# Performance work log

Measured on AMD Instinct MI355X. Metric: run time of the kernel, lower is better.

The kernel has to match this reference:

```python
import jax, jax.numpy as jnp
import numpy as np

TEMP = 0.07
BASE_TEMP = 0.07
BANK = 8192
B = 512      # samples per view; features has 2*B rows
D = 128      # feature dim
N_CLASSES = 100


def _l2norm(x, axis=-1):
    return x / jnp.linalg.norm(x, axis=axis, keepdims=True)


def setup_inputs() -> dict:
    key = jax.random.key(0)
    k1, k2, k3, k4, k5 = jax.random.split(key, 5)
    # SupCon features are L2-normalized embeddings; two views stacked: [2B, 1, D]
    features = _l2norm(jax.random.normal(k1, (2 * B, 1, D), jnp.float32))
    label = jax.random.randint(k2, (B,), 0, N_CLASSES)
    # memory banks stored as [D, bank_size] (lightly MemoryBankModule layout)
    bank1 = _l2norm(jax.random.normal(k3, (D, BANK), jnp.float32), axis=0)
    bank2 = _l2norm(jax.random.normal(k4, (D, BANK), jnp.float32), axis=0)
    bank_labels = jax.random.randint(k5, (BANK,), 0, N_CLASSES)
    return {"features": features, "label": label, "bank1": bank1,
            "bank2": bank2, "bank_labels": bank_labels}


def _branch_loss(cf, pos_mask, neg_mask):
    # cf: [N, D] anchor==contrast features
    logits = jnp.matmul(cf, cf.T) / TEMP                       # [N, N]
    logits = logits - jax.lax.stop_gradient(logits.max(axis=1, keepdims=True))
    # denominator: sum of exp(logits) over NEGATIVES only (square(mask-1) mask)
    denom = jnp.log((jnp.exp(logits) * neg_mask).sum(axis=1, keepdims=True))
    log_prob = logits - denom                                  # [N, N]
    mean_log_prob_pos = (pos_mask * log_prob).sum(axis=1) / pos_mask.sum(axis=1)
    return -(TEMP / BASE_TEMP) * mean_log_prob_pos             # [N]


def reference(features, label, bank1, bank2, bank_labels):
    d = features.shape[-1]
    fr = features.reshape(-1, d)                # [2B, D]
    nb = fr.shape[0] // 2
    f1, f2 = fr[:nb], fr[nb:]                   # [B, D] each

    labels_all = jnp.concatenate([bank_labels.reshape(-1, 1),
                                  label.reshape(-1, 1)], axis=0)   # [N, 1]
    same = (labels_all == labels_all.T)                            # [N, N]
    mask = same.astype(fr.dtype)
    n = mask.shape[0]
    self_mask = 1.0 - jnp.eye(n, dtype=fr.dtype)
    pos_mask = mask * self_mask                 # positives excluding self
    neg_mask = jnp.square(mask - 1.0)           # 1 where labels differ

    cf1 = jnp.concatenate([bank2.T, f1], axis=0)   # [N, D]
    cf2 = jnp.concatenate([bank1.T, f2], axis=0)   # [N, D]

    class_loss = (_branch_loss(cf1, pos_mask, neg_mask)
                  + _branch_loss(cf2, pos_mask, neg_mask)) / 2.0
    loss = class_loss.mean()
    return (loss, loss, loss)
```

## Files before the change

kernel.cpp:

```cpp
#include <hip/hip_runtime.h>
#include <math.h>

#define NTOT 8704
#define BANKN 8192
#define NB 512
#define DIM 128
#define INVT (1.0f / 0.07f)
#define C2L 20.6099131801f
#define NCHUNK 17
#define TPC 8
#define BN 64

using short8 = __attribute__((ext_vector_type(8))) short;
using ushort8 = __attribute__((ext_vector_type(8))) unsigned short;
using f32x4 = __attribute__((ext_vector_type(4))) float;

static __device__ __forceinline__ ushort f2bf(float f) {
  union { float f; unsigned u; } v;
  v.f = f;
  unsigned r = v.u + 0x7fffu + ((v.u >> 16) & 1u);
  return (ushort)(r >> 16);
}

static __device__ __forceinline__ float fast_exp2(float x) {
#if __has_builtin(__builtin_amdgcn_exp2f)
  return __builtin_amdgcn_exp2f(x);
#else
  return exp2f(x);
#endif
}

__global__ __launch_bounds__(1024) void prep_kernel(
    const int* __restrict__ bank_labels, const int* __restrict__ label,
    int* __restrict__ inv, int* __restrict__ lo, int* __restrict__ hi,
    float* __restrict__ zp) {
  __shared__ int h[101];
  __shared__ int st[101];
  __shared__ int cur[100];
  const int tid = threadIdx.x;
  for (int i = tid; i < NTOT; i += 1024)
    reinterpret_cast<float4*>(zp)[i] = make_float4(0.f, 0.f, 0.f, 0.f);
  if (tid < 101) h[tid] = 0;
  __syncthreads();
  for (int i = tid; i < NTOT; i += 1024) {
    const int v = (i < BANKN) ? bank_labels[i] : label[i - BANKN];
    atomicAdd(&h[v], 1);
  }
  __syncthreads();
  if (tid == 0) {
    int s = 0;
    for (int c = 0; c < 100; ++c) { st[c] = s; s += h[c]; }
    st[100] = s;
  }
  __syncthreads();
  if (tid < 100) cur[tid] = st[tid];
  __syncthreads();
  for (int i = tid; i < NTOT; i += 1024) {
    const int v = (i < BANKN) ? bank_labels[i] : label[i - BANKN];
    const int p = atomicAdd(&cur[v], 1);
    inv[i] = p;
    lo[p] = st[v];
    hi[p] = st[v + 1];
  }
}

__global__ void pack_kernel(const float* __restrict__ features,
                            const float* __restrict__ bank1,
                            const float* __restrict__ bank2,
                            const int* __restrict__ inv,
                            ushort* __restrict__ cf1b,
                            ushort* __restrict__ cf2b) {
  const int branch = blockIdx.z;
  ushort* __restrict__ dst = branch ? cf2b : cf1b;
  const int tx = threadIdx.x, ty = threadIdx.y;
  const int bx = blockIdx.x, by = blockIdx.y;
  if (bx < 256) {
    const float* __restrict__ src = branch ? bank1 : bank2;
    __shared__ float tile[32][33];
    const int col = bx * 32 + tx;
#pragma unroll
    for (int s = 0; s < 32; s += 8)
      tile[ty + s][tx] = src[(size_t)(by * 32 + ty + s) * BANKN + col];
    __syncthreads();
    const int k = by * 32 + tx;
#pragma unroll
    for (int s = 0; s < 32; s += 8) {
      const int p = inv[bx * 32 + ty + s];
      dst[(size_t)p * DIM + k] = f2bf(tile[tx][ty + s]);
    }
  } else {
    const int j = (bx - 256) * 32 + ty;
#pragma unroll
    for (int s = 0; s < 32; s += 8) {
      const int jr = (bx - 256) * 32 + ty + s;
      const int k = by * 32 + tx;
      const float v = features[(size_t)(branch * NB + jr) * DIM + k];
      const int p = inv[BANKN + jr];
      dst[(size_t)p * DIM + k] = f2bf(v);
    }
    (void)j;
  }
}

__global__ __launch_bounds__(256) void supcon_mfma_kernel(
    const ushort* __restrict__ cf1b, const ushort* __restrict__ cf2b,
    const int* __restrict__ lo, const int* __restrict__ hi,
    float* __restrict__ zp) {
  const int rb = blockIdx.x;
  const int chunk = blockIdx.y;
  const int branch = blockIdx.z;
  const ushort* __restrict__ cf = branch ? cf2b : cf1b;

  const int tid = threadIdx.x;
  const int wid = tid >> 6, lane = tid & 63;
  const int l15 = lane & 15, l4 = lane >> 4;
  const int rowW = rb * 128 + wid * 32;

  __shared__ ushort Bt[2][BN * DIM];

  short8 a[2][4];
#pragma unroll
  for (int rt = 0; rt < 2; ++rt) {
    const int r = rowW + rt * 16 + l15;
#pragma unroll
    for (int ks = 0; ks < 4; ++ks)
      a[rt][ks] = *reinterpret_cast<const short8*>(cf + (size_t)r * DIM + ks * 32 + l4 * 8);
  }
  int rlo[2][4], rhi[2][4];
#pragma unroll
  for (int rt = 0; rt < 2; ++rt)
#pragma unroll
    for (int rg = 0; rg < 4; ++rg) {
      const int rr = rowW + rt * 16 + l4 * 4 + rg;
      rlo[rt][rg] = lo[rr];
      rhi[rt][rg] = hi[rr];
    }
  const int u_lo = lo[rowW];
  const int u_hi = hi[rowW + 31];
  const int lo_last = lo[rowW + 31];
  const int hi_first = hi[rowW];

  float Zr[2][4] = {{0.f, 0.f, 0.f, 0.f}, {0.f, 0.f, 0.f, 0.f}};
  float Pr[2][4] = {{0.f, 0.f, 0.f, 0.f}, {0.f, 0.f, 0.f, 0.f}};

  auto STAGE = [&](int t, int buf) {
    const int col0 = (chunk * TPC + t) * BN;
#pragma unroll
    for (int it = 0; it < 4; ++it) {
      const int o = it * 256 + tid;
      const int row = o >> 4, cc = o & 15;
      const ushort* src =
          cf + (size_t)(col0 + row) * DIM + ((cc ^ (row & 7)) * 8);
      ushort* dst = &Bt[buf][(it * 256 + wid * 64) * 8];
      __builtin_amdgcn_global_load_lds(
          (const __attribute__((address_space(1))) void*)src,
          (__attribute__((address_space(3))) void*)dst, 16, 0, 0);
    }
  };

  STAGE(0, 0);
  asm volatile("s_waitcnt vmcnt(0)" ::: "memory");
  __syncthreads();

  int cur = 0;
  for (int t = 0; t < TPC; ++t) {
    if (t + 1 < TPC) STAGE(t + 1, cur ^ 1);

    const int col0 = (chunk * TPC + t) * BN;

    f32x4 acc[2][4];
#pragma unroll
    for (int rt = 0; rt < 2; ++rt)
#pragma unroll
      for (int ct = 0; ct < 4; ++ct) acc[rt][ct] = (f32x4){0.f, 0.f, 0.f, 0.f};

#pragma unroll
    for (int ks = 0; ks < 4; ++ks) {
      short8 b[4];
#pragma unroll
      for (int ct = 0; ct < 4; ++ct) {
        const int r = ct * 16 + l15;
        const int swz = (ks * 4 + l4) ^ (r & 7);
        b[ct] = *reinterpret_cast<const short8*>(&Bt[cur][r * DIM + swz * 8]);
      }
#pragma unroll
      for (int rt = 0; rt < 2; ++rt)
#pragma unroll
        for (int ct = 0; ct < 4; ++ct)
          acc[rt][ct] = __builtin_amdgcn_mfma_f32_16x16x32_bf16(
              a[rt][ks], b[ct], acc[rt][ct], 0, 0, 0);
    }

    if (col0 + BN <= u_lo || col0 >= u_hi) {
#pragma unroll
      for (int ct = 0; ct < 4; ++ct)
#pragma unroll
        for (int rt = 0; rt < 2; ++rt)
#pragma unroll
          for (int rg = 0; rg < 4; ++rg)
            Zr[rt][rg] += fast_exp2(fmaf(acc[rt][ct][rg], C2L, -C2L));
    } else if (col0 >= lo_last && col0 + BN <= hi_first) {
#pragma unroll
      for (int ct = 0; ct < 4; ++ct)
#pragma unroll
        for (int rt = 0; rt < 2; ++rt)
#pragma unroll
          for (int rg = 0; rg < 4; ++rg) Pr[rt][rg] += acc[rt][ct][rg];
    } else {
#pragma unroll
      for (int ct = 0; ct < 4; ++ct) {
        const int c = col0 + ct * 16 + l15;
#pragma unroll
        for (int rt = 0; rt < 2; ++rt)
#pragma unroll
          for (int rg = 0; rg < 4; ++rg) {
            const float v = acc[rt][ct][rg];
            const float e = fast_exp2(fmaf(v, C2L, -C2L));
            const bool s = (c >= rlo[rt][rg]) && (c < rhi[rt][rg]);
            Zr[rt][rg] += s ? 0.0f : e;
            Pr[rt][rg] += s ? v : 0.0f;
          }
      }
    }

    asm volatile("s_waitcnt vmcnt(0)" ::: "memory");
    __syncthreads();
    cur ^= 1;
  }

  float* Zrow = zp;
  float* Prow = zp + 2 * NTOT;
#pragma unroll
  for (int rt = 0; rt < 2; ++rt)
#pragma unroll
    for (int rg = 0; rg < 4; ++rg) {
      float z = Zr[rt][rg], p = Pr[rt][rg];
#pragma unroll
      for (int off = 1; off < 16; off <<= 1) {
        z += __shfl_xor(z, off);
        p += __shfl_xor(p, off);
      }
      if (l15 == 0) {
        const int row = rowW + rt * 16 + l4 * 4 + rg;
        atomicAdd(&Zrow[branch * NTOT + row], z);
        atomicAdd(&Prow[branch * NTOT + row], p);
      }
    }
}

__global__ __launch_bounds__(1024) void loss_kernel(const float* __restrict__ zp,
                                                    const int* __restrict__ lo,
                                                    const int* __restrict__ hi,
                                                    float* __restrict__ out) {
  const int tid = threadIdx.x;
  const float* Zrow = zp;
  const float* Prow = zp + 2 * NTOT;
  float local = 0.f;
  for (int idx = tid; idx < 2 * NTOT; idx += 1024) {
    const int row = (idx >= NTOT) ? idx - NTOT : idx;
    const float z = Zrow[idx];
    const float p = Prow[idx];
    const float C = (float)(hi[row] - lo[row] - 1);
    const float denom = INVT + logf(z);
    local += -((INVT * (p - 1.0f)) / C - denom);
  }
  __shared__ float s[1024];
  s[tid] = local;
  __syncthreads();
  for (int st = 512; st > 0; st >>= 1) {
    if (tid < st) s[tid] += s[tid + st];
    __syncthreads();
  }
  if (tid == 0) {
    const float v = s[0] / (2.0f * NTOT);
    out[0] = v; out[1] = v; out[2] = v;
  }
}

extern "C" void kernel_launch(void* const* d_in, const int* in_sizes, int n_in,
                              void* d_out, int out_size, void* d_ws,
                              size_t ws_size, hipStream_t stream) {
  const float* features = (const float*)d_in[0];
  const int* label = (const int*)d_in[1];
  const float* bank1 = (const float*)d_in[2];
  const float* bank2 = (const float*)d_in[3];
  const int* bank_labels = (const int*)d_in[4];
  float* out = (float*)d_out;

  char* ws = (char*)d_ws;
  ushort* cf1b = (ushort*)(ws);
  ushort* cf2b = (ushort*)(ws + 2228224);
  int* inv = (int*)(ws + 4456448);
  int* lo = (int*)(ws + 4491264);
  int* hi = (int*)(ws + 4526080);
  float* zp = (float*)(ws + 4560896);

  prep_kernel<<<dim3(1), dim3(1024), 0, stream>>>(bank_labels, label, inv, lo,
                                                  hi, zp);
  pack_kernel<<<dim3(272, DIM / 32, 2), dim3(32, 8), 0, stream>>>(
      features, bank1, bank2, inv, cf1b, cf2b);
  supcon_mfma_kernel<<<dim3(NTOT / 128, NCHUNK, 2), dim3(256), 0, stream>>>(
      cf1b, cf2b, lo, hi, zp);
  loss_kernel<<<dim3(1), dim3(1024), 0, stream>>>(zp, lo, hi, out);
}
```

Baseline: 154.0 us.

## Triple-buffer MFMA tiles, use 2x2 wave grid, and privatize label histograms

The main kernel moves from double to triple buffering with one barrier per tile and a partial vmcnt wait, so the load for tile t+2 is in flight while tile t is computed. Waves now form a 2x2 grid of 64 rows by 32 columns, which lowers LDS B-fragment reads per MFMA. Label bounds now live in shared memory instead of registers, the LDS swizzle widens to 16, and launch bounds request 3 blocks per SM. The prep kernel uses per-wave histograms to reduce atomic contention, at the cost of more LDS and a small prefix step.

```diff
diff --git a/kernel.cpp b/kernel.cpp
--- a/kernel.cpp
+++ b/kernel.cpp
@@ -34,30 +34,46 @@
     const int* __restrict__ bank_labels, const int* __restrict__ label,
     int* __restrict__ inv, int* __restrict__ lo, int* __restrict__ hi,
     float* __restrict__ zp) {
-  __shared__ int h[101];
+  __shared__ int h[16][100];
   __shared__ int st[101];
-  __shared__ int cur[100];
+  __shared__ int tot[100];
   const int tid = threadIdx.x;
+  const int w = tid >> 6;
   for (int i = tid; i < NTOT; i += 1024)
     reinterpret_cast<float4*>(zp)[i] = make_float4(0.f, 0.f, 0.f, 0.f);
-  if (tid < 101) h[tid] = 0;
+  for (int i = tid; i < 1600; i += 1024) (&h[0][0])[i] = 0;
   __syncthreads();
   for (int i = tid; i < NTOT; i += 1024) {
     const int v = (i < BANKN) ? bank_labels[i] : label[i - BANKN];
-    atomicAdd(&h[v], 1);
+    atomicAdd(&h[w][v], 1);
+  }
+  __syncthreads();
+  if (tid < 100) {
+    int s = 0;
+#pragma unroll
+    for (int w2 = 0; w2 < 16; ++w2) s += h[w2][tid];
+    tot[tid] = s;
   }
   __syncthreads();
   if (tid == 0) {
     int s = 0;
-    for (int c = 0; c < 100; ++c) { st[c] = s; s += h[c]; }
+    for (int c = 0; c < 100; ++c) { st[c] = s; s += tot[c]; }
     st[100] = s;
   }
   __syncthreads();
-  if (tid < 100) cur[tid] = st[tid];
+  if (tid < 100) {
+    int base = st[tid];
+#pragma unroll
+    for (int w2 = 0; w2 < 16; ++w2) {
+      const int t = h[w2][tid];
+      h[w2][tid] = base;
+      base += t;
+    }
+  }
   __syncthreads();
   for (int i = tid; i < NTOT; i += 1024) {
     const int v = (i < BANKN) ? bank_labels[i] : label[i - BANKN];
-    const int p = atomicAdd(&cur[v], 1);
+    const int p = atomicAdd(&h[w][v], 1);
     inv[i] = p;
     lo[p] = st[v];
     hi[p] = st[v + 1];
@@ -89,7 +105,6 @@
       dst[(size_t)p * DIM + k] = f2bf(tile[tx][ty + s]);
     }
   } else {
-    const int j = (bx - 256) * 32 + ty;
 #pragma unroll
     for (int s = 0; s < 32; s += 8) {
       const int jr = (bx - 256) * 32 + ty + s;
@@ -98,11 +113,10 @@
       const int p = inv[BANKN + jr];
       dst[(size_t)p * DIM + k] = f2bf(v);
     }
-    (void)j;
-  }
-}
-
-__global__ __launch_bounds__(256) void supcon_mfma_kernel(
+  }
+}
+
+__global__ __launch_bounds__(256, 3) void supcon_mfma_kernel(
     const ushort* __restrict__ cf1b, const ushort* __restrict__ cf2b,
     const int* __restrict__ lo, const int* __restrict__ hi,
     float* __restrict__ zp) {
@@ -114,34 +128,33 @@
   const int tid = threadIdx.x;
   const int wid = tid >> 6, lane = tid & 63;
   const int l15 = lane & 15, l4 = lane >> 4;
-  const int rowW = rb * 128 + wid * 32;
-
-  __shared__ ushort Bt[2][BN * DIM];
-
-  short8 a[2][4];
-#pragma unroll
-  for (int rt = 0; rt < 2; ++rt) {
+  const int wr = wid >> 1, wc = wid & 1;
+  const int rowB = rb * 128;
+  const int rowW = rowB + wr * 64;
+
+  __shared__ ushort Bt[3][BN * DIM];
+  __shared__ int sLo[128], sHi[128];
+
+  if (tid < 128) {
+    sLo[tid] = lo[rowB + tid];
+    sHi[tid] = hi[rowB + tid];
+  }
+
+  short8 a[4][4];
+#pragma unroll
+  for (int rt = 0; rt < 4; ++rt) {
     const int r = rowW + rt * 16 + l15;
 #pragma unroll
     for (int ks = 0; ks < 4; ++ks)
       a[rt][ks] = *reinterpret_cast<const short8*>(cf + (size_t)r * DIM + ks * 32 + l4 * 8);
   }
-  int rlo[2][4], rhi[2][4];
-#pragma unroll
-  for (int rt = 0; rt < 2; ++rt)
-#pragma unroll
-    for (int rg = 0; rg < 4; ++rg) {
-      const int rr = rowW + rt * 16 + l4 * 4 + rg;
-      rlo[rt][rg] = lo[rr];
-      rhi[rt][rg] = hi[rr];
-    }
   const int u_lo = lo[rowW];
-  const int u_hi = hi[rowW + 31];
-  const int lo_last = lo[rowW + 31];
+  const int u_hi = hi[rowW + 63];
+  const int lo_last = lo[rowW + 63];
   const int hi_first = hi[rowW];
 
-  float Zr[2][4] = {{0.f, 0.f, 0.f, 0.f}, {0.f, 0.f, 0.f, 0.f}};
-  float Pr[2][4] = {{0.f, 0.f, 0.f, 0.f}, {0.f, 0.f, 0.f, 0.f}};
+  float Zr[4][4] = {};
+  float Pr[4][4] = {};
 
   auto STAGE = [&](int t, int buf) {
     const int col0 = (chunk * TPC + t) * BN;
@@ -150,7 +163,7 @@
       const int o = it * 256 + tid;
       const int row = o >> 4, cc = o & 15;
       const ushort* src =
-          cf + (size_t)(col0 + row) * DIM + ((cc ^ (row & 7)) * 8);
+          cf + (size_t)(col0 + row) * DIM + ((cc ^ (row & 15)) * 8);
       ushort* dst = &Bt[buf][(it * 256 + wid * 64) * 8];
       __builtin_amdgcn_global_load_lds(
           (const __attribute__((address_space(1))) void*)src,
@@ -159,79 +172,83 @@
   };
 
   STAGE(0, 0);
-  asm volatile("s_waitcnt vmcnt(0)" ::: "memory");
-  __syncthreads();
-
-  int cur = 0;
+  STAGE(1, 1);
+
   for (int t = 0; t < TPC; ++t) {
-    if (t + 1 < TPC) STAGE(t + 1, cur ^ 1);
+    if (t + 1 < TPC)
+      asm volatile("s_waitcnt vmcnt(4)" ::: "memory");
+    else
+      asm volatile("s_waitcnt vmcnt(0)" ::: "memory");
+    __syncthreads();
+    if (t + 2 < TPC) STAGE(t + 2, (t + 2) % 3);
 
     const int col0 = (chunk * TPC + t) * BN;
-
-    f32x4 acc[2][4];
-#pragma unroll
-    for (int rt = 0; rt < 2; ++rt)
-#pragma unroll
-      for (int ct = 0; ct < 4; ++ct) acc[rt][ct] = (f32x4){0.f, 0.f, 0.f, 0.f};
-
+    const ushort* __restrict__ B = &Bt[t % 3][0];
+
+    f32x4 acc[4][2];
+#pragma unroll
+    for (int rt = 0; rt < 4; ++rt)
+#pragma unroll
+      for (int ct = 0; ct < 2; ++ct) acc[rt][ct] = (f32x4){0.f, 0.f, 0.f, 0.f};
+
+    __builtin_amdgcn_s_setprio(1);
 #pragma unroll
     for (int ks = 0; ks < 4; ++ks) {
-      short8 b[4];
-#pragma unroll
-      for (int ct = 0; ct < 4; ++ct) {
-        const int r = ct * 16 + l15;
-        const int swz = (ks * 4 + l4) ^ (r & 7);
-        b[ct] = *reinterpret_cast<const short8*>(&Bt[cur][r * DIM + swz * 8]);
+      short8 b[2];
+#pragma unroll
+      for (int ct = 0; ct < 2; ++ct) {
+        const int r = wc * 32 + ct * 16 + l15;
+        const int swz = (ks * 4 + l4) ^ (r & 15);
+        b[ct] = *reinterpret_cast<const short8*>(&B[r * DIM + swz * 8]);
       }
 #pragma unroll
-      for (int rt = 0; rt < 2; ++rt)
-#pragma unroll
-        for (int ct = 0; ct < 4; ++ct)
+      for (int rt = 0; rt < 4; ++rt)
+#pragma unroll
+        for (int ct = 0; ct < 2; ++ct)
           acc[rt][ct] = __builtin_amdgcn_mfma_f32_16x16x32_bf16(
               a[rt][ks], b[ct], acc[rt][ct], 0, 0, 0);
     }
-
-    if (col0 + BN <= u_lo || col0 >= u_hi) {
-#pragma unroll
-      for (int ct = 0; ct < 4; ++ct)
-#pragma unroll
-        for (int rt = 0; rt < 2; ++rt)
+    __builtin_amdgcn_s_setprio(0);
+
+    const int wcol0 = col0 + wc * 32;
+    if (wcol0 + 32 <= u_lo || wcol0 >= u_hi) {
+#pragma unroll
+      for (int ct = 0; ct < 2; ++ct)
+#pragma unroll
+        for (int rt = 0; rt < 4; ++rt)
 #pragma unroll
           for (int rg = 0; rg < 4; ++rg)
             Zr[rt][rg] += fast_exp2(fmaf(acc[rt][ct][rg], C2L, -C2L));
-    } else if (col0 >= lo_last && col0 + BN <= hi_first) {
-#pragma unroll
-      for (int ct = 0; ct < 4; ++ct)
-#pragma unroll
-        for (int rt = 0; rt < 2; ++rt)
+    } else if (wcol0 >= lo_last && wcol0 + 32 <= hi_first) {
+#pragma unroll
+      for (int ct = 0; ct < 2; ++ct)
+#pragma unroll
+        for (int rt = 0; rt < 4; ++rt)
 #pragma unroll
           for (int rg = 0; rg < 4; ++rg) Pr[rt][rg] += acc[rt][ct][rg];
     } else {
 #pragma unroll
-      for (int ct = 0; ct < 4; ++ct) {
-        const int c = col0 + ct * 16 + l15;
-#pragma unroll
-        for (int rt = 0; rt < 2; ++rt)
+      for (int ct = 0; ct < 2; ++ct) {
+        const int c = wcol0 + ct * 16 + l15;
+#pragma unroll
+        for (int rt = 0; rt < 4; ++rt)
 #pragma unroll
           for (int rg = 0; rg < 4; ++rg) {
+            const int rloc = wr * 64 + rt * 16 + l4 * 4 + rg;
             const float v = acc[rt][ct][rg];
             const float e = fast_exp2(fmaf(v, C2L, -C2L));
-            const bool s = (c >= rlo[rt][rg]) && (c < rhi[rt][rg]);
+            const bool s = (c >= sLo[rloc]) && (c < sHi[rloc]);
             Zr[rt][rg] += s ? 0.0f : e;
             Pr[rt][rg] += s ? v : 0.0f;
           }
       }
     }
-
-    asm volatile("s_waitcnt vmcnt(0)" ::: "memory");
-    __syncthreads();
-    cur ^= 1;
   }
 
   float* Zrow = zp;
   float* Prow = zp + 2 * NTOT;
 #pragma unroll
-  for (int rt = 0; rt < 2; ++rt)
+  for (int rt = 0; rt < 4; ++rt)
 #pragma unroll
     for (int rg = 0; rg < 4; ++rg) {
       float z = Zr[rt][rg], p = Pr[rt][rg];
```

After: 198.9 us. +29.2%, slower.
